# Kernel optimization log

Measured on AMD Instinct MI355X. Metric: run time of the kernel, lower is better.

The kernel has to match this reference:

```python
import jax, jax.numpy as jnp
import numpy as np

EPS = 1e-16

def setup_inputs() -> dict:
    key = jax.random.key(0)
    k1, k2, k3, k4, k5, k6 = jax.random.split(key, 6)
    B, S, NT, E = 8, 256, 50, 64
    # sorted event times in [0, 90); horizon T = 100 > all events; all valid (>=0)
    event_times = jnp.sort(jax.random.uniform(k1, (B, S), dtype=jnp.float32) * 90.0, axis=1)
    event_types = jax.random.randint(k2, (B, S), 0, NT)
    # parameters initialized N(0, 0.1) as in _initialize_parameters
    type_embeddings = 0.1 * jax.random.normal(k3, (NT, E), dtype=jnp.float32)
    a = 0.1 * jax.random.normal(k4, (NT, E), dtype=jnp.float32)
    A = 0.1 * jax.random.normal(k5, (NT, NT, E), dtype=jnp.float32)
    P = 0.1 * jax.random.normal(k6, (NT, NT, E), dtype=jnp.float32)
    return {"event_times": event_times, "event_types": event_types, "T": 100,
            "type_embeddings": type_embeddings, "a": a, "A": A, "P": P}

def _hawkes_nll(event_times, event_types, T, emb, a, A, P):
    B, S = event_times.shape
    NT, E = emb.shape
    Tf = jnp.asarray(T, jnp.float32)
    emb_t = emb[event_types]            # (B,S,E) embedding of each event's type
    a_t = a[event_types]                # (B,S,E)
    valid = event_times >= 0.0          # (B,S)

    # ---- log-likelihood: intensity of the observed type at each event time ----
    # pairwise: axis 1 = query event i, axis 2 = history event j (j < i)
    dt = event_times[:, :, None] - event_times[:, None, :]                 # (B,Si,Sj)
    hist_mask = (jnp.arange(S)[:, None] > jnp.arange(S)[None, :])[None]    # (1,Si,Sj): j<i
    # A_pair[b,i,j,e] = A[type_j, type_i, e]; same for P_pair
    A_pair = A[event_types[:, None, :], event_types[:, :, None]]           # (B,Si,Sj,E)
    P_pair = P[event_types[:, None, :], event_types[:, :, None]]
    emb_i = emb_t[:, :, None, :]                                           # (B,Si,1,E)
    emb_j = emb_t[:, None, :, :]                                           # (B,1,Sj,E)
    decay = jnp.exp(-(emb_i * P_pair) * emb_j * dt[..., None])
    contrib = (emb_i * A_pair) * decay * emb_j                             # (B,Si,Sj,E)
    m = jnp.sum(jnp.where(hist_mask[..., None], contrib, 0.0), axis=2)     # (B,Si,E)
    inten = jnp.sum(jax.nn.softplus(emb_t * a_t + m), axis=-1)             # (B,S)
    ll = jnp.sum(jnp.where(valid, jnp.log(inten + EPS), 0.0))

    # ---- integral approximation (as in compute_loss) ----
    # intensity at horizon T for ALL types, using full valid history
    dT = Tf - event_times                                                  # (B,S)
    A_all = A[event_types]                                                 # (B,S,NT,E): A[t_j, t, e]
    P_all = P[event_types]
    decT = jnp.exp(-(emb[None, None] * P_all) * emb_t[:, :, None, :] * dT[:, :, None, None])
    conT = (emb[None, None] * A_all) * decT * emb_t[:, :, None, :]         # (B,S,NT,E)
    m_T = jnp.sum(jnp.where(valid[:, :, None, None], conT, 0.0), axis=1)   # (B,NT,E)
    inten_T = jnp.sum(jax.nn.softplus(emb * a + m_T), axis=(-2, -1))       # (B,)

    base_sum = jnp.sum(jax.nn.softplus(emb * a))                           # empty-history intensity summed over types
    any_valid = jnp.any(valid, axis=1)                                     # (B,)
    last_time = jnp.where(any_valid, jnp.max(jnp.where(valid, event_times, -1e30), axis=1), 0.0)
    first_time = jnp.where(any_valid, jnp.min(jnp.where(valid, event_times, 1e30), axis=1), 0.0)
    integ_b = jnp.where(any_valid,
                        inten_T * (Tf - last_time) + base_sum * first_time,
                        base_sum * Tf)
    integral = jnp.sum(integ_b)
    return -(ll - integral)

def reference(event_times, event_types, T, type_embeddings, a, A, P):
    return _hawkes_nll(event_times, event_types, T, type_embeddings, a, A, P)
```

## Files before the change

### kernel.cpp

```cpp
#include <hip/hip_runtime.h>
#include <math.h>

#define B   8
#define S   256
#define NT  50
#define E   64
#define NTE (NT * E)
#define EPSF 1e-16f
#define LOG2E 1.4426950408889634f

#define NW        8
#define NTHREADS  (64 * NW)
#define LL_BLOCKS (B * S / 2)
#define IN_BLOCKS (B * NT)

__device__ __forceinline__ float softplus(float x) {
    if (x > 20.0f) return x;
    return log1pf(__expf(x));
}

__device__ __forceinline__ float wave_reduce_sum(float v) {
    #pragma unroll
    for (int off = 32; off > 0; off >>= 1)
        v += __shfl_down(v, off, 64);
    return v;
}

__global__ __launch_bounds__(NTHREADS) void main_kernel(
    const float* __restrict__ times, const int* __restrict__ types,
    const int* __restrict__ Tp,
    const float* __restrict__ emb,  const float* __restrict__ a,
    const float* __restrict__ Amat, const float* __restrict__ Pmat,
    float* __restrict__ ws_ll, float* __restrict__ ws_int)
{
    const int tid = threadIdx.x;
    const int e   = tid & 63;
    const int w   = tid >> 6;
    const int bid = blockIdx.x;
    const bool is_ll = (bid < LL_BLOCKS);
    const int b = is_ll ? (bid / (S / 2)) : ((bid - LL_BLOCKS) / NT);

    __shared__ __align__(16) float  s_emb[NTE];
    __shared__ __align__(16) float2 s_AP[2][NTE];
    __shared__ float2 s_ev[S];
    __shared__ float  s_part[2][NW][E];
    __shared__ float  s_row[2];

    int ty0, ty1;
    if (is_ll) {
        const int ih = bid % (S / 2);
        ty0 = types[b * S + ih];
        ty1 = types[b * S + (S - 1 - ih)];
    } else {
        ty0 = (bid - LL_BLOCKS) % NT;
        ty1 = ty0;
    }

    {
        const float4* __restrict__ emb4 = (const float4*)emb;
        float4* s4 = (float4*)s_emb;
        for (int idx = tid; idx < NTE / 4; idx += NTHREADS)
            s4[idx] = emb4[idx];
    }
    for (int idx = tid; idx < NTE; idx += NTHREADS) {
        const int row = idx >> 6, col = idx & 63;
        const int g0 = row * NTE + ty0 * E + col;
        s_AP[0][idx] = make_float2(Amat[g0], Pmat[g0]);
        if (is_ll) {
            const int g1 = row * NTE + ty1 * E + col;
            s_AP[1][idx] = make_float2(Amat[g1], Pmat[g1]);
        }
    }
    for (int j = tid; j < S; j += NTHREADS)
        s_ev[j] = make_float2(times[b * S + j],
                              __int_as_float(types[b * S + j] * E));
    __syncthreads();

    if (is_ll) {
        const int ih = bid % (S / 2);
        const int rows[2] = { ih, S - 1 - ih };
        #pragma unroll
        for (int r = 0; r < 2; ++r) {
            const int   i      = rows[r];
            const float t_i    = s_ev[i].x;
            const int   col    = __float_as_int(s_ev[i].y) + e;
            const float negEi2 = -s_emb[col] * LOG2E;

            float macc = 0.0f;
            #pragma unroll 8
            for (int j = w; j < i; j += NW) {
                const float2 ev   = s_ev[j];
                const float  dtj  = t_i - ev.x;
                const int    sidx = __float_as_int(ev.y) + e;
                const float  ej   = s_emb[sidx];
                const float2 ap   = s_AP[r][sidx];
                macc = fmaf(ap.x * ej, exp2f(negEi2 * ap.y * ej * dtj), macc);
            }
            s_part[r][w][e] = macc;
        }
        __syncthreads();
        if (w < 2) {
            const int   i     = rows[w];
            const float t_i   = s_ev[i].x;
            const int   col   = __float_as_int(s_ev[i].y) + e;
            const float emb_i = s_emb[col];
            float mt = 0.0f;
            #pragma unroll
            for (int q = 0; q < NW; ++q) mt += s_part[w][q][e];
            const float sp    = softplus(fmaf(emb_i, mt, emb_i * a[col]));
            const float inten = wave_reduce_sum(sp);
            if (e == 0)
                s_row[w] = (t_i >= 0.0f) ? logf(inten + EPSF) : 0.0f;
        }
        __syncthreads();
        if (tid == 0) ws_ll[bid] = s_row[0] + s_row[1];
    } else {
        const float Tf     = (float)(*Tp);
        const int   colk   = ty0 * E + e;
        const float embk   = s_emb[colk];
        const float negEk2 = -embk * LOG2E;

        float acc = 0.0f;
        #pragma unroll 8
        for (int i = w; i < S; i += NW) {
            const float2 ev   = s_ev[i];
            const float  dT   = Tf - ev.x;
            const int    sidx = __float_as_int(ev.y) + e;
            const float  et   = s_emb[sidx];
            const float2 ap   = s_AP[0][sidx];
            const float  c    = ap.x * et * exp2f(negEk2 * ap.y * et * dT);
            acc += (ev.x >= 0.0f) ? c : 0.0f;
        }
        s_part[0][w][e] = acc;
        __syncthreads();
        if (w == 0) {
            float mt = 0.0f;
            #pragma unroll
            for (int q = 0; q < NW; ++q) mt += s_part[0][q][e];
            const float sp = softplus(fmaf(embk, mt, embk * a[colk]));
            const float s  = wave_reduce_sum(sp);
            if (e == 0) ws_int[bid - LL_BLOCKS] = s;
        }
    }
}

__global__ __launch_bounds__(256) void finalize_kernel(
    const float* __restrict__ times,
    const int* __restrict__ Tp,
    const float* __restrict__ emb, const float* __restrict__ a,
    const float* __restrict__ ws_ll, const float* __restrict__ ws_int,
    float* __restrict__ out)
{
    const int t    = threadIdx.x;
    const int lane = t & 63;
    const int w    = t >> 6;
    const float Tf = (float)(*Tp);

    float llp = 0.0f;
    for (int idx = t; idx < LL_BLOCKS; idx += 256) llp += ws_ll[idx];
    float bs = 0.0f;
    for (int idx = t; idx < NTE; idx += 256) bs += softplus(emb[idx] * a[idx]);

    __shared__ float red[256], red2[256];
    red[t] = llp; red2[t] = bs;

    __shared__ float s_first[B], s_last[B], s_iT[B], s_any[B];
    for (int b = w; b < B; b += 4) {
        float mn = 1e30f, mx = -1e30f;
        #pragma unroll
        for (int q = 0; q < S / 64; ++q) {
            const float tv = times[b * S + q * 64 + lane];
            const bool valid = (tv >= 0.0f);
            mn = fminf(mn, valid ? tv : 1e30f);
            mx = fmaxf(mx, valid ? tv : -1e30f);
        }
        float iv = (lane < NT) ? ws_int[b * NT + lane] : 0.0f;
        #pragma unroll
        for (int off = 32; off > 0; off >>= 1) {
            mn = fminf(mn, __shfl_down(mn, off, 64));
            mx = fmaxf(mx, __shfl_down(mx, off, 64));
            iv += __shfl_down(iv, off, 64);
        }
        if (lane == 0) {
            const bool any_valid = (mn < 1e29f);
            s_any[b]   = any_valid ? 1.0f : 0.0f;
            s_first[b] = any_valid ? mn : 0.0f;
            s_last[b]  = any_valid ? mx : 0.0f;
            s_iT[b]    = iv;
        }
    }
    __syncthreads();

    for (int off = 128; off > 0; off >>= 1) {
        if (t < off) { red[t] += red[t + off]; red2[t] += red2[t + off]; }
        __syncthreads();
    }

    if (t == 0) {
        const float base_sum = red2[0];
        float integral = 0.0f;
        #pragma unroll
        for (int b = 0; b < B; ++b) {
            integral += (s_any[b] > 0.5f)
                ? s_iT[b] * (Tf - s_last[b]) + base_sum * s_first[b]
                : base_sum * Tf;
        }
        out[0] = integral - red[0];
    }
}

extern "C" void kernel_launch(void* const* d_in, const int* in_sizes, int n_in,
                              void* d_out, int out_size, void* d_ws, size_t ws_size,
                              hipStream_t stream) {
    const float* times = (const float*)d_in[0];
    const int*   types = (const int*)d_in[1];
    const int*   Tp    = (const int*)d_in[2];
    const float* emb   = (const float*)d_in[3];
    const float* a     = (const float*)d_in[4];
    const float* Amat  = (const float*)d_in[5];
    const float* Pmat  = (const float*)d_in[6];

    float* ws     = (float*)d_ws;
    float* ws_ll  = ws;
    float* ws_int = ws + LL_BLOCKS;
    float* out    = (float*)d_out;

    main_kernel<<<LL_BLOCKS + IN_BLOCKS, NTHREADS, 0, stream>>>(
        times, types, Tp, emb, a, Amat, Pmat, ws_ll, ws_int);
    finalize_kernel<<<1, 256, 0, stream>>>(times, Tp, emb, a, ws_ll, ws_int, out);
}
```

Measured before the change: 98.00 us.

## Precompute interleaved A*emb, P*emb table and read it from global instead of LDS staging

Result: faster. 91.90 us (-6.2%).

```diff
diff --git a/kernel.cpp b/kernel.cpp
--- a/kernel.cpp
+++ b/kernel.cpp
@@ -9,10 +9,11 @@
 #define EPSF 1e-16f
 #define LOG2E 1.4426950408889634f
 
-#define NW        8
+#define NW        4
 #define NTHREADS  (64 * NW)
 #define LL_BLOCKS (B * S / 2)
 #define IN_BLOCKS (B * NT)
+#define TAB_ELEMS (NT * NTE)
 
 __device__ __forceinline__ float softplus(float x) {
     if (x > 20.0f) return x;
@@ -26,11 +27,22 @@
     return v;
 }
 
+__global__ __launch_bounds__(256) void pre_kernel(
+    const float* __restrict__ emb,
+    const float* __restrict__ Amat, const float* __restrict__ Pmat,
+    float2* __restrict__ tab)
+{
+    const int i   = blockIdx.x * 256 + threadIdx.x;
+    const int tyj = i / NTE;
+    const float ej = emb[tyj * E + (i & 63)];
+    tab[i] = make_float2(Amat[i] * ej, Pmat[i] * ej);
+}
+
 __global__ __launch_bounds__(NTHREADS) void main_kernel(
     const float* __restrict__ times, const int* __restrict__ types,
     const int* __restrict__ Tp,
     const float* __restrict__ emb,  const float* __restrict__ a,
-    const float* __restrict__ Amat, const float* __restrict__ Pmat,
+    const float2* __restrict__ tab,
     float* __restrict__ ws_ll, float* __restrict__ ws_int)
 {
     const int tid = threadIdx.x;
@@ -40,40 +52,16 @@
     const bool is_ll = (bid < LL_BLOCKS);
     const int b = is_ll ? (bid / (S / 2)) : ((bid - LL_BLOCKS) / NT);
 
-    __shared__ __align__(16) float  s_emb[NTE];
-    __shared__ __align__(16) float2 s_AP[2][NTE];
-    __shared__ float2 s_ev[S];
-    __shared__ float  s_part[2][NW][E];
-    __shared__ float  s_row[2];
-
-    int ty0, ty1;
-    if (is_ll) {
-        const int ih = bid % (S / 2);
-        ty0 = types[b * S + ih];
-        ty1 = types[b * S + (S - 1 - ih)];
-    } else {
-        ty0 = (bid - LL_BLOCKS) % NT;
-        ty1 = ty0;
-    }
-
-    {
-        const float4* __restrict__ emb4 = (const float4*)emb;
-        float4* s4 = (float4*)s_emb;
-        for (int idx = tid; idx < NTE / 4; idx += NTHREADS)
-            s4[idx] = emb4[idx];
-    }
-    for (int idx = tid; idx < NTE; idx += NTHREADS) {
-        const int row = idx >> 6, col = idx & 63;
-        const int g0 = row * NTE + ty0 * E + col;
-        s_AP[0][idx] = make_float2(Amat[g0], Pmat[g0]);
-        if (is_ll) {
-            const int g1 = row * NTE + ty1 * E + col;
-            s_AP[1][idx] = make_float2(Amat[g1], Pmat[g1]);
-        }
-    }
-    for (int j = tid; j < S; j += NTHREADS)
-        s_ev[j] = make_float2(times[b * S + j],
-                              __int_as_float(types[b * S + j] * E));
+    __shared__ __align__(16) float4 s_ev[S];
+    __shared__ float s_part[2][NW][E];
+    __shared__ float s_row[2];
+
+    for (int j = tid; j < S; j += NTHREADS) {
+        const int ty = types[b * S + j];
+        s_ev[j] = make_float4(times[b * S + j],
+                              __int_as_float(ty * E),
+                              __int_as_float(ty * NTE), 0.0f);
+    }
     __syncthreads();
 
     if (is_ll) {
@@ -84,17 +72,16 @@
             const int   i      = rows[r];
             const float t_i    = s_ev[i].x;
             const int   col    = __float_as_int(s_ev[i].y) + e;
-            const float negEi2 = -s_emb[col] * LOG2E;
+            const float negEi2 = -emb[col] * LOG2E;
 
             float macc = 0.0f;
             #pragma unroll 8
             for (int j = w; j < i; j += NW) {
-                const float2 ev   = s_ev[j];
-                const float  dtj  = t_i - ev.x;
-                const int    sidx = __float_as_int(ev.y) + e;
-                const float  ej   = s_emb[sidx];
-                const float2 ap   = s_AP[r][sidx];
-                macc = fmaf(ap.x * ej, exp2f(negEi2 * ap.y * ej * dtj), macc);
+                const float4 ev  = s_ev[j];
+                const float  dtj = t_i - ev.x;
+                const int    idx = __float_as_int(ev.z) + col;
+                const float2 ap  = tab[idx];
+                macc = fmaf(ap.x, exp2f(negEi2 * ap.y * dtj), macc);
             }
             s_part[r][w][e] = macc;
         }
@@ -103,7 +90,7 @@
             const int   i     = rows[w];
             const float t_i   = s_ev[i].x;
             const int   col   = __float_as_int(s_ev[i].y) + e;
-            const float emb_i = s_emb[col];
+            const float emb_i = emb[col];
             float mt = 0.0f;
             #pragma unroll
             for (int q = 0; q < NW; ++q) mt += s_part[w][q][e];
@@ -115,20 +102,20 @@
         __syncthreads();
         if (tid == 0) ws_ll[bid] = s_row[0] + s_row[1];
     } else {
+        const int   k      = (bid - LL_BLOCKS) % NT;
         const float Tf     = (float)(*Tp);
-        const int   colk   = ty0 * E + e;
-        const float embk   = s_emb[colk];
+        const int   colk   = k * E + e;
+        const float embk   = emb[colk];
         const float negEk2 = -embk * LOG2E;
 
         float acc = 0.0f;
         #pragma unroll 8
         for (int i = w; i < S; i += NW) {
-            const float2 ev   = s_ev[i];
-            const float  dT   = Tf - ev.x;
-            const int    sidx = __float_as_int(ev.y) + e;
-            const float  et   = s_emb[sidx];
-            const float2 ap   = s_AP[0][sidx];
-            const float  c    = ap.x * et * exp2f(negEk2 * ap.y * et * dT);
+            const float4 ev  = s_ev[i];
+            const float  dT  = Tf - ev.x;
+            const int    idx = __float_as_int(ev.z) + colk;
+            const float2 ap  = tab[idx];
+            const float  c   = ap.x * exp2f(negEk2 * ap.y * dT);
             acc += (ev.x >= 0.0f) ? c : 0.0f;
         }
         s_part[0][w][e] = acc;
@@ -220,12 +207,14 @@
     const float* Amat  = (const float*)d_in[5];
     const float* Pmat  = (const float*)d_in[6];
 
-    float* ws     = (float*)d_ws;
-    float* ws_ll  = ws;
-    float* ws_int = ws + LL_BLOCKS;
-    float* out    = (float*)d_out;
-
+    float*  ws     = (float*)d_ws;
+    float*  ws_ll  = ws;
+    float*  ws_int = ws + LL_BLOCKS;
+    float2* tab    = (float2*)(ws + 2048);
+    float*  out    = (float*)d_out;
+
+    pre_kernel<<<TAB_ELEMS / 256, 256, 0, stream>>>(emb, Amat, Pmat, tab);
     main_kernel<<<LL_BLOCKS + IN_BLOCKS, NTHREADS, 0, stream>>>(
-        times, types, Tp, emb, a, Amat, Pmat, ws_ll, ws_int);
+        times, types, Tp, emb, a, tab, ws_ll, ws_int);
     finalize_kernel<<<1, 256, 0, stream>>>(times, Tp, emb, a, ws_ll, ws_int, out);
 }
```
